# Optimization experiments

Hardware: AMD Instinct MI355X
Metric: run time of the kernel (lower is better)

## Reference

```python
import jax, jax.numpy as jnp
import numpy as np

B, N, C, H, W, V = 2, 8, 64, 192, 256, 200000
R = N * H * W
OUT = 128


def setup_inputs() -> dict:
    key = jax.random.key(0)
    k = jax.random.split(key, 8)
    camera_pose = jnp.eye(4, dtype=jnp.float32) + 0.1 * jax.random.normal(k[0], (B, N, 4, 4), dtype=jnp.float32)
    intr = jnp.array([200.0, 200.0, W / 2.0, H / 2.0, float(W), float(H)], dtype=jnp.float32)
    padded_intrinsics = jnp.broadcast_to(intr, (B, N, 6))
    padded_img_features = jax.random.normal(k[1], (B, N, C, H, W), dtype=jnp.float32)
    depths = jax.random.uniform(k[2], (B, N, H, W), dtype=jnp.float32)
    padding_confidence = jax.random.uniform(k[3], (B, V, 1), dtype=jnp.float32)
    voxel_ids = jax.random.randint(k[4], (B, R), 0, V).astype(jnp.int32)
    hit_mask = jax.random.bernoulli(k[5], 0.5, (B, R))
    w_fc = 0.02 * jax.random.normal(k[6], (C + 1, OUT), dtype=jnp.float32)
    b_fc = 0.01 * jax.random.normal(k[7], (OUT,), dtype=jnp.float32)
    return {"camera_pose": camera_pose, "padded_intrinsics": padded_intrinsics,
            "padded_img_features": padded_img_features, "depths": depths,
            "padding_confidence": padding_confidence, "voxel_ids": voxel_ids,
            "hit_mask": hit_mask, "w_fc": w_fc, "b_fc": b_fc}


def _rays(pose, intr):
    # pose: [B,N,4,4], intr: [B,N,6] = fx,fy,cx,cy,w,h
    fx, fy, cx, cy = intr[..., 0], intr[..., 1], intr[..., 2], intr[..., 3]
    ii, jj = jnp.meshgrid(jnp.arange(W, dtype=intr.dtype), jnp.arange(H, dtype=intr.dtype), indexing="xy")  # [H,W]
    uu = (ii - cx[..., None, None]) / fx[..., None, None]  # [B,N,H,W]
    vv = (jj - cy[..., None, None]) / fy[..., None, None]
    ones = jnp.ones_like(uu)
    local = jnp.stack([uu, vv, ones, ones], axis=-1)  # [B,N,H,W,4]
    pixel_xyz = jnp.einsum("bnij,bnhwj->bnhwi", pose, local)[..., :3]
    origin = pose[..., :3, 3]  # [B,N,3]
    d = pixel_xyz - origin[:, :, None, None, :]
    d = d / jnp.linalg.norm(d, axis=-1, keepdims=True)
    return origin, d


def _scatter_mean(x, ids, mask):
    # x: [R,C]; ids: [R]; mask: [R] bool. Non-hit rays routed to dummy segment V.
    seg = jnp.where(mask, ids, V)
    sums = jax.ops.segment_sum(x, seg, num_segments=V + 1)[:V]
    cnt = jax.ops.segment_sum(mask.astype(x.dtype), seg, num_segments=V + 1)[:V]
    return sums / jnp.maximum(cnt, 1.0)[:, None]  # voxels with no hits stay zero


def reference(camera_pose, padded_intrinsics, padded_img_features, depths,
              padding_confidence, voxel_ids, hit_mask, w_fc, b_fc):
    origins, d = _rays(camera_pose, padded_intrinsics)
    # [B,N,C,H,W] -> [B, N*H*W, C]  (matches permute(0,2,3,1).view(N*H*W,-1) per batch)
    x = jnp.transpose(padded_img_features, (0, 1, 3, 4, 2)).reshape(B, R, C)
    vox = jax.vmap(_scatter_mean)(x, voxel_ids, hit_mask)  # [B,V,C]
    vox = jnp.concatenate([vox, padding_confidence], axis=-1)  # [B,V,C+1]
    out = vox @ w_fc + b_fc  # mix_fc
    return out, d
```

## Files before the change

kernel.cpp:

```cpp
#include <hip/hip_runtime.h>
#include <hip/hip_bf16.h>

#define B_ 2
#define N_ 8
#define C_ 64
#define H_ 192
#define W_ 256
#define V_ 200000
#define OUT_ 128
#define HW_ (H_*W_)
#define R_ (N_*HW_)
#define BV_ (B_*V_)
#define BR_ (B_*R_)
#define SCAN_E 2048
#define SCAN_BLOCKS ((BV_ + SCAN_E - 1)/SCAN_E)

__global__ __launch_bounds__(256) void ray_kernel(
    const float* __restrict__ pose,
    const float* __restrict__ intr,
    float* __restrict__ dout)
{
    const int blocksPerBN = HW_ / 256;
    int tid = threadIdx.x;
    int bn = blockIdx.x / blocksPerBN;
    int hw = (blockIdx.x % blocksPerBN) * 256 + tid;
    int h = hw / W_, w = hw % W_;

    __shared__ float p[12];
    __shared__ float it[4];
    if (tid < 12) p[tid] = pose[bn * 16 + tid];
    if (tid >= 12 && tid < 16) it[tid - 12] = intr[bn * 6 + (tid - 12)];
    __syncthreads();

    float fx = it[0], fy = it[1], cx = it[2], cy = it[3];
    float uu = ((float)w - cx) / fx;
    float vv = ((float)h - cy) / fy;
    float dx = p[0] * uu + p[1] * vv + p[2];
    float dy = p[4] * uu + p[5] * vv + p[6];
    float dz = p[8] * uu + p[9] * vv + p[10];
    float inv = rsqrtf(dx * dx + dy * dy + dz * dz);
    size_t o = (size_t)(bn * HW_ + hw) * 3;
    dout[o + 0] = dx * inv;
    dout[o + 1] = dy * inv;
    dout[o + 2] = dz * inv;
}

__global__ __launch_bounds__(256) void hist_kernel(
    const int* __restrict__ vox,
    const int* __restrict__ hit,
    unsigned* __restrict__ hist)
{
    int t = blockIdx.x * 256 + threadIdx.x;
    if (t >= BR_) return;
    int b = t / R_;
    if (hit[t]) atomicAdd(&hist[b * V_ + vox[t]], 1u);
}

__global__ __launch_bounds__(256) void scanA_kernel(
    const unsigned* __restrict__ hist,
    unsigned* __restrict__ blockSums)
{
    int tid = threadIdx.x;
    int base = blockIdx.x * SCAN_E + tid * 8;
    unsigned s = 0;
    #pragma unroll
    for (int j = 0; j < 8; ++j) {
        int idx = base + j;
        if (idx < BV_) s += hist[idx];
    }
    __shared__ unsigned sh[256];
    sh[tid] = s; __syncthreads();
    for (int d = 128; d > 0; d >>= 1) {
        if (tid < d) sh[tid] += sh[tid + d];
        __syncthreads();
    }
    if (tid == 0) blockSums[blockIdx.x] = sh[0];
}

__global__ __launch_bounds__(256) void scanB_kernel(
    const unsigned* __restrict__ blockSums,
    unsigned* __restrict__ blockOffsets)
{
    int tid = threadIdx.x;
    unsigned v = (tid < SCAN_BLOCKS) ? blockSums[tid] : 0u;
    __shared__ unsigned sh[256];
    sh[tid] = v; __syncthreads();
    for (int d = 1; d < 256; d <<= 1) {
        unsigned t = (tid >= d) ? sh[tid - d] : 0u;
        __syncthreads();
        sh[tid] += t;
        __syncthreads();
    }
    if (tid < SCAN_BLOCKS) blockOffsets[tid] = sh[tid] - v;
}

__global__ __launch_bounds__(256) void scanC_kernel(
    const unsigned* __restrict__ hist,
    const unsigned* __restrict__ blockOffsets,
    unsigned* __restrict__ offsets)
{
    int tid = threadIdx.x;
    int base = blockIdx.x * SCAN_E + tid * 8;
    unsigned e[8];
    unsigned s = 0;
    #pragma unroll
    for (int j = 0; j < 8; ++j) {
        int idx = base + j;
        e[j] = (idx < BV_) ? hist[idx] : 0u;
        s += e[j];
    }
    __shared__ unsigned sh[256];
    sh[tid] = s; __syncthreads();
    for (int d = 1; d < 256; d <<= 1) {
        unsigned t = (tid >= d) ? sh[tid - d] : 0u;
        __syncthreads();
        sh[tid] += t;
        __syncthreads();
    }
    unsigned run = blockOffsets[blockIdx.x] + (sh[tid] - s);
    #pragma unroll
    for (int j = 0; j < 8; ++j) {
        int idx = base + j;
        if (idx < BV_) offsets[idx] = run;
        run += e[j];
    }
}

__global__ __launch_bounds__(256) void scatterfeat_kernel(
    const float* __restrict__ feat,
    const int* __restrict__ vox,
    const int* __restrict__ hit,
    const unsigned* __restrict__ offsets,
    unsigned* __restrict__ offs2,
    float* __restrict__ gathered,
    int b0)
{
    int t = blockIdx.x * 256 + threadIdx.x;
    int p = b0 * R_ + t;
    if (!hit[p]) return;
    int b = p / R_;
    int r = p - b * R_;
    unsigned base = offsets[(size_t)b0 * V_];
    int key = b * V_ + vox[p];
    unsigned pos = atomicAdd(&offs2[key], 1u) - base;

    int n = r / HW_;
    int hw = r - n * HW_;
    const float* fb = feat + ((size_t)b * N_ + n) * (size_t)(C_ * HW_) + hw;

    float v[64];
    #pragma unroll
    for (int c = 0; c < 64; ++c) v[c] = fb[(size_t)c * HW_];

    float4* gp = (float4*)(gathered + (size_t)pos * 64);
    #pragma unroll
    for (int q = 0; q < 16; ++q) {
        float4 st; st.x = v[4*q]; st.y = v[4*q+1]; st.z = v[4*q+2]; st.w = v[4*q+3];
        gp[q] = st;
    }
}

__global__ __launch_bounds__(256) void gemm_fused_kernel(
    const float* __restrict__ gathered,
    const unsigned* __restrict__ hist,
    const unsigned* __restrict__ offsets,
    const float* __restrict__ conf,
    const float* __restrict__ wfc,
    const float* __restrict__ bfc,
    float* __restrict__ outp,
    int b0)
{
    const int VPB = 32;
    __shared__ float wl[65][128];
    __shared__ float voxT[65][36];
    __shared__ float bl[128];
    int tid = threadIdx.x;
    int bv0 = b0 * V_ + blockIdx.x * VPB;
    unsigned base = offsets[(size_t)b0 * V_];

    for (int i = tid; i < 65 * 128; i += 256)
        wl[i >> 7][i & 127] = wfc[i];
    if (tid < 128) bl[tid] = bfc[tid];
    if (tid < VPB) voxT[64][tid] = conf[bv0 + tid];

    int lane = tid & 63;
    int wv = tid >> 6;
    #pragma unroll
    for (int i = 0; i < 8; ++i) {
        int lv = wv * 8 + i;
        int bv = bv0 + lv;
        unsigned cnt = hist[bv];
        unsigned st = offsets[bv] - base;
        float acc = 0.0f;
        for (unsigned k = 0; k < cnt; ++k)
            acc += gathered[(size_t)(st + k) * 64 + lane];
        voxT[lane][lv] = acc / fmaxf((float)cnt, 1.0f);
    }
    __syncthreads();

    int oc = tid & 31;
    int vr = tid >> 5;
    float acc[4][4];
    float4 bq = *(float4*)&bl[oc * 4];
    #pragma unroll
    for (int i = 0; i < 4; ++i) {
        acc[i][0] = bq.x; acc[i][1] = bq.y; acc[i][2] = bq.z; acc[i][3] = bq.w;
    }

    #pragma unroll
    for (int c = 0; c < 65; ++c) {
        float4 v4 = *(float4*)&voxT[c][vr * 4];
        float4 w4 = *(float4*)&wl[c][oc * 4];
        acc[0][0] += v4.x * w4.x; acc[0][1] += v4.x * w4.y; acc[0][2] += v4.x * w4.z; acc[0][3] += v4.x * w4.w;
        acc[1][0] += v4.y * w4.x; acc[1][1] += v4.y * w4.y; acc[1][2] += v4.y * w4.z; acc[1][3] += v4.y * w4.w;
        acc[2][0] += v4.z * w4.x; acc[2][1] += v4.z * w4.y; acc[2][2] += v4.z * w4.z; acc[2][3] += v4.z * w4.w;
        acc[3][0] += v4.w * w4.x; acc[3][1] += v4.w * w4.y; acc[3][2] += v4.w * w4.z; acc[3][3] += v4.w * w4.w;
    }

    #pragma unroll
    for (int i = 0; i < 4; ++i) {
        size_t bv = (size_t)(bv0 + vr * 4 + i);
        float4 st;
        st.x = acc[i][0]; st.y = acc[i][1]; st.z = acc[i][2]; st.w = acc[i][3];
        *(float4*)&outp[bv * OUT_ + oc * 4] = st;
    }
}

__global__ __launch_bounds__(256) void scatter_kernel(
    const float* __restrict__ feat,
    const int* __restrict__ vox_ids,
    const int* __restrict__ hit,
    float* __restrict__ sums,
    unsigned* __restrict__ cnts)
{
    const int PPT = 2;
    const int blocksPerBN = HW_ / (256 * PPT);
    int tid = threadIdx.x;
    int bn = blockIdx.x / blocksPerBN;
    int b = bn >> 3;
    int hw0 = (blockIdx.x % blocksPerBN) * (256 * PPT) + tid * PPT;
    int r0 = (bn & 7) * HW_ + hw0;

    int2 vid = *(const int2*)(vox_ids + (size_t)b * R_ + r0);
    int2 ht  = *(const int2*)(hit + (size_t)b * R_ + r0);
    if (!(ht.x | ht.y)) return;

    unsigned* cb = cnts + (size_t)b * V_;
    if (ht.x) atomicAdd(&cb[vid.x], 1u);
    if (ht.y) atomicAdd(&cb[vid.y], 1u);

    float* sb = sums + (size_t)b * (size_t)V_ * C_;
    float* s0 = sb + (size_t)vid.x * C_;
    float* s1 = sb + (size_t)vid.y * C_;
    const float* fb = feat + (size_t)bn * C_ * HW_ + hw0;

    #pragma unroll 8
    for (int c = 0; c < C_; ++c) {
        float2 rw = *(const float2*)(fb + (size_t)c * HW_);
        if (ht.x) unsafeAtomicAdd(s0 + c, rw.x);
        if (ht.y) unsafeAtomicAdd(s1 + c, rw.y);
    }
}

__global__ __launch_bounds__(256) void gemm_atomic_kernel(
    const float* __restrict__ sums,
    const unsigned* __restrict__ cnts,
    const float* __restrict__ conf,
    const float* __restrict__ wfc,
    const float* __restrict__ bfc,
    float* __restrict__ outp)
{
    const int VPB = 32;
    __shared__ float wl[65][128];
    __shared__ float voxT[65][36];
    __shared__ float bl[128];
    __shared__ float invc[VPB];
    int tid = threadIdx.x;
    int bv0 = blockIdx.x * VPB;

    for (int i = tid; i < 65 * 128; i += 256)
        wl[i >> 7][i & 127] = wfc[i];
    if (tid < 128) bl[tid] = bfc[tid];
    if (tid < VPB) {
        unsigned cn = cnts[bv0 + tid];
        invc[tid] = 1.0f / (float)(cn > 1u ? cn : 1u);
        voxT[64][tid] = conf[bv0 + tid];
    }
    __syncthreads();

    for (int i = tid; i < VPB * C_; i += 256) {
        int vx = i >> 6, c = i & 63;
        voxT[c][vx] = sums[(size_t)bv0 * C_ + i] * invc[vx];
    }
    __syncthreads();

    int oc = tid & 31;
    int vr = tid >> 5;
    float acc[4][4];
    float4 bq = *(float4*)&bl[oc * 4];
    #pragma unroll
    for (int i = 0; i < 4; ++i) {
        acc[i][0] = bq.x; acc[i][1] = bq.y; acc[i][2] = bq.z; acc[i][3] = bq.w;
    }

    #pragma unroll
    for (int c = 0; c < 65; ++c) {
        float4 v4 = *(float4*)&voxT[c][vr * 4];
        float4 w4 = *(float4*)&wl[c][oc * 4];
        acc[0][0] += v4.x * w4.x; acc[0][1] += v4.x * w4.y; acc[0][2] += v4.x * w4.z; acc[0][3] += v4.x * w4.w;
        acc[1][0] += v4.y * w4.x; acc[1][1] += v4.y * w4.y; acc[1][2] += v4.y * w4.z; acc[1][3] += v4.y * w4.w;
        acc[2][0] += v4.z * w4.x; acc[2][1] += v4.z * w4.y; acc[2][2] += v4.z * w4.z; acc[2][3] += v4.z * w4.w;
        acc[3][0] += v4.w * w4.x; acc[3][1] += v4.w * w4.y; acc[3][2] += v4.w * w4.z; acc[3][3] += v4.w * w4.w;
    }

    #pragma unroll
    for (int i = 0; i < 4; ++i) {
        size_t bv = (size_t)(bv0 + vr * 4 + i);
        float4 st;
        st.x = acc[i][0]; st.y = acc[i][1]; st.z = acc[i][2]; st.w = acc[i][3];
        *(float4*)&outp[bv * OUT_ + oc * 4] = st;
    }
}

extern "C" void kernel_launch(void* const* d_in, const int* in_sizes, int n_in,
                              void* d_out, int out_size, void* d_ws, size_t ws_size,
                              hipStream_t stream) {
    const float* pose = (const float*)d_in[0];
    const float* intr = (const float*)d_in[1];
    const float* feat = (const float*)d_in[2];
    const float* conf = (const float*)d_in[4];
    const int* vox_ids = (const int*)d_in[5];
    const int* hit = (const int*)d_in[6];
    const float* wfc = (const float*)d_in[7];
    const float* bfc = (const float*)d_in[8];

    float* out = (float*)d_out;
    float* dray = out + (size_t)B_ * V_ * OUT_;

    ray_kernel<<<(B_ * N_ * HW_) / 256, 256, 0, stream>>>(pose, intr, dray);

    size_t hist_bytes = (size_t)BV_ * sizeof(unsigned);
    size_t gath_full  = (size_t)BR_ * C_ * sizeof(float);
    size_t gath_batch = (size_t)R_ * C_ * sizeof(float);
    size_t ovh = 3 * hist_bytes + 512 * sizeof(unsigned);
    size_t need_full  = gath_full + ovh;
    size_t need_batch = gath_batch + ovh;

    if (ws_size >= need_batch) {
        size_t gath_bytes = (ws_size >= need_full) ? gath_full : gath_batch;
        float* gathered = (float*)d_ws;
        unsigned* hist = (unsigned*)((char*)d_ws + gath_bytes);
        unsigned* offsets = hist + BV_;
        unsigned* offs2 = offsets + BV_;
        unsigned* blockSums = offs2 + BV_;
        unsigned* blockOffsets = blockSums + 256;

        hipMemsetAsync(hist, 0, hist_bytes, stream);
        hist_kernel<<<BR_ / 256, 256, 0, stream>>>(vox_ids, hit, hist);
        scanA_kernel<<<SCAN_BLOCKS, 256, 0, stream>>>(hist, blockSums);
        scanB_kernel<<<1, 256, 0, stream>>>(blockSums, blockOffsets);
        scanC_kernel<<<SCAN_BLOCKS, 256, 0, stream>>>(hist, blockOffsets, offsets);
        hipMemcpyAsync(offs2, offsets, hist_bytes, hipMemcpyDeviceToDevice, stream);

        if (ws_size >= need_full) {
            scatterfeat_kernel<<<BR_ / 256, 256, 0, stream>>>(feat, vox_ids, hit, offsets, offs2, gathered, 0);
            gemm_fused_kernel<<<BV_ / 32, 256, 0, stream>>>(gathered, hist, offsets, conf, wfc, bfc, out, 0);
        } else {
            for (int b = 0; b < B_; ++b) {
                scatterfeat_kernel<<<R_ / 256, 256, 0, stream>>>(feat, vox_ids, hit, offsets, offs2, gathered, b);
                gemm_fused_kernel<<<V_ / 32, 256, 0, stream>>>(gathered, hist, offsets, conf, wfc, bfc, out, b);
            }
        }
    } else {
        float* sums = (float*)d_ws;
        size_t sums_bytes = (size_t)B_ * V_ * C_ * sizeof(float);
        unsigned* cnts = (unsigned*)((char*)d_ws + sums_bytes);
        size_t cnts_bytes = (size_t)B_ * V_ * sizeof(unsigned);

        hipMemsetAsync(d_ws, 0, sums_bytes + cnts_bytes, stream);
        scatter_kernel<<<(B_ * N_ * HW_) / (256 * 2), 256, 0, stream>>>(feat, vox_ids, hit, sums, cnts);
        gemm_atomic_kernel<<<(B_ * V_) / 32, 256, 0, stream>>>(sums, cnts, conf, wfc, bfc, out);
    }
}
```

Baseline: 621.2 us.

## Process two rays per thread in scatter, widen GEMM tile, fuse offset copy

The offsets copy is folded into the scan kernel, removing a separate device-to-device memcpy. The feature scatter now handles two adjacent pixels per thread with float2 loads in four channel chunks, which cuts per-thread register pressure and halves the hit/vox index loads. The fused mean+GEMM kernel moves from 32 to 64 voxels per block, issues the segment loads for eight voxels at a time to raise memory parallelism, and streams the weights through shared memory in 22-row chunks to hold LDS use down. The cost is extra synchronisation for the weight reloads and more accumulator registers per thread.

```diff
diff --git a/kernel.cpp b/kernel.cpp
--- a/kernel.cpp
+++ b/kernel.cpp
@@ -97,7 +97,8 @@
 __global__ __launch_bounds__(256) void scanC_kernel(
     const unsigned* __restrict__ hist,
     const unsigned* __restrict__ blockOffsets,
-    unsigned* __restrict__ offsets)
+    unsigned* __restrict__ offsets,
+    unsigned* __restrict__ offs2)
 {
     int tid = threadIdx.x;
     int base = blockIdx.x * SCAN_E + tid * 8;
@@ -121,7 +122,7 @@
     #pragma unroll
     for (int j = 0; j < 8; ++j) {
         int idx = base + j;
-        if (idx < BV_) offsets[idx] = run;
+        if (idx < BV_) { offsets[idx] = run; offs2[idx] = run; }
         run += e[j];
     }
 }
@@ -136,27 +137,45 @@
     int b0)
 {
     int t = blockIdx.x * 256 + threadIdx.x;
-    int p = b0 * R_ + t;
-    if (!hit[p]) return;
-    int b = p / R_;
-    int r = p - b * R_;
+    int p0 = b0 * R_ + t * 2;
+    int2 ht = *(const int2*)(hit + p0);
+    if (!(ht.x | ht.y)) return;
+    int2 vd = *(const int2*)(vox + p0);
+    int b = p0 / R_;
+    int r0 = p0 - b * R_;
     unsigned base = offsets[(size_t)b0 * V_];
-    int key = b * V_ + vox[p];
-    unsigned pos = atomicAdd(&offs2[key], 1u) - base;
-
-    int n = r / HW_;
-    int hw = r - n * HW_;
+    unsigned px = 0, py = 0;
+    if (ht.x) px = atomicAdd(&offs2[b * V_ + vd.x], 1u) - base;
+    if (ht.y) py = atomicAdd(&offs2[b * V_ + vd.y], 1u) - base;
+
+    int n = r0 / HW_;
+    int hw = r0 - n * HW_;
     const float* fb = feat + ((size_t)b * N_ + n) * (size_t)(C_ * HW_) + hw;
-
-    float v[64];
-    #pragma unroll
-    for (int c = 0; c < 64; ++c) v[c] = fb[(size_t)c * HW_];
-
-    float4* gp = (float4*)(gathered + (size_t)pos * 64);
-    #pragma unroll
-    for (int q = 0; q < 16; ++q) {
-        float4 st; st.x = v[4*q]; st.y = v[4*q+1]; st.z = v[4*q+2]; st.w = v[4*q+3];
-        gp[q] = st;
+    float* gx = gathered + (size_t)px * 64;
+    float* gy = gathered + (size_t)py * 64;
+
+    #pragma unroll 1
+    for (int ch = 0; ch < 4; ++ch) {
+        float2 v[16];
+        #pragma unroll
+        for (int j = 0; j < 16; ++j)
+            v[j] = *(const float2*)(fb + (size_t)(ch * 16 + j) * HW_);
+        if (ht.x) {
+            #pragma unroll
+            for (int q = 0; q < 4; ++q) {
+                float4 s;
+                s.x = v[4*q].x; s.y = v[4*q+1].x; s.z = v[4*q+2].x; s.w = v[4*q+3].x;
+                *(float4*)(gx + ch * 16 + q * 4) = s;
+            }
+        }
+        if (ht.y) {
+            #pragma unroll
+            for (int q = 0; q < 4; ++q) {
+                float4 s;
+                s.x = v[4*q].y; s.y = v[4*q+1].y; s.z = v[4*q+2].y; s.w = v[4*q+3].y;
+                *(float4*)(gy + ch * 16 + q * 4) = s;
+            }
+        }
     }
 }
 
@@ -170,59 +189,88 @@
     float* __restrict__ outp,
     int b0)
 {
-    const int VPB = 32;
-    __shared__ float wl[65][128];
-    __shared__ float voxT[65][36];
+    const int VPB = 64;
+    const int KC = 22;
+    __shared__ float wl[KC][128];
+    __shared__ float voxT[66][68];
     __shared__ float bl[128];
     int tid = threadIdx.x;
     int bv0 = b0 * V_ + blockIdx.x * VPB;
     unsigned base = offsets[(size_t)b0 * V_];
 
-    for (int i = tid; i < 65 * 128; i += 256)
-        wl[i >> 7][i & 127] = wfc[i];
     if (tid < 128) bl[tid] = bfc[tid];
     if (tid < VPB) voxT[64][tid] = conf[bv0 + tid];
+    if (tid < 68)  voxT[65][tid] = 0.0f;
 
     int lane = tid & 63;
     int wv = tid >> 6;
-    #pragma unroll
-    for (int i = 0; i < 8; ++i) {
-        int lv = wv * 8 + i;
-        int bv = bv0 + lv;
-        unsigned cnt = hist[bv];
-        unsigned st = offsets[bv] - base;
-        float acc = 0.0f;
-        for (unsigned k = 0; k < cnt; ++k)
-            acc += gathered[(size_t)(st + k) * 64 + lane];
-        voxT[lane][lv] = acc / fmaxf((float)cnt, 1.0f);
-    }
+    for (int g = 0; g < 2; ++g) {
+        unsigned cn[8], st[8];
+        float macc[8];
+        #pragma unroll
+        for (int i = 0; i < 8; ++i) {
+            int bv = bv0 + wv * 16 + g * 8 + i;
+            cn[i] = hist[bv];
+            st[i] = offsets[bv] - base;
+        }
+        #pragma unroll
+        for (int i = 0; i < 8; ++i)
+            macc[i] = cn[i] ? gathered[(size_t)st[i] * 64 + lane] : 0.0f;
+        #pragma unroll
+        for (int i = 0; i < 8; ++i)
+            for (unsigned k = 1; k < cn[i]; ++k)
+                macc[i] += gathered[(size_t)(st[i] + k) * 64 + lane];
+        #pragma unroll
+        for (int i = 0; i < 8; ++i)
+            voxT[lane][wv * 16 + g * 8 + i] = macc[i] / fmaxf((float)cn[i], 1.0f);
+    }
+
+    for (int i = tid; i < KC * 128; i += 256)
+        wl[i >> 7][i & 127] = wfc[i];
     __syncthreads();
 
     int oc = tid & 31;
     int vr = tid >> 5;
-    float acc[4][4];
+    float acc[8][4];
     float4 bq = *(float4*)&bl[oc * 4];
     #pragma unroll
-    for (int i = 0; i < 4; ++i) {
+    for (int i = 0; i < 8; ++i) {
         acc[i][0] = bq.x; acc[i][1] = bq.y; acc[i][2] = bq.z; acc[i][3] = bq.w;
     }
 
-    #pragma unroll
-    for (int c = 0; c < 65; ++c) {
-        float4 v4 = *(float4*)&voxT[c][vr * 4];
-        float4 w4 = *(float4*)&wl[c][oc * 4];
-        acc[0][0] += v4.x * w4.x; acc[0][1] += v4.x * w4.y; acc[0][2] += v4.x * w4.z; acc[0][3] += v4.x * w4.w;
-        acc[1][0] += v4.y * w4.x; acc[1][1] += v4.y * w4.y; acc[1][2] += v4.y * w4.z; acc[1][3] += v4.y * w4.w;
-        acc[2][0] += v4.z * w4.x; acc[2][1] += v4.z * w4.y; acc[2][2] += v4.z * w4.z; acc[2][3] += v4.z * w4.w;
-        acc[3][0] += v4.w * w4.x; acc[3][1] += v4.w * w4.y; acc[3][2] += v4.w * w4.z; acc[3][3] += v4.w * w4.w;
-    }
-
-    #pragma unroll
-    for (int i = 0; i < 4; ++i) {
-        size_t bv = (size_t)(bv0 + vr * 4 + i);
-        float4 st;
-        st.x = acc[i][0]; st.y = acc[i][1]; st.z = acc[i][2]; st.w = acc[i][3];
-        *(float4*)&outp[bv * OUT_ + oc * 4] = st;
+    for (int h = 0; h < 3; ++h) {
+        int c0 = h * KC;
+        #pragma unroll
+        for (int cl = 0; cl < KC; ++cl) {
+            int c = c0 + cl;
+            float4 va = *(float4*)&voxT[c][vr * 8];
+            float4 vb = *(float4*)&voxT[c][vr * 8 + 4];
+            float4 w4 = *(float4*)&wl[cl][oc * 4];
+            acc[0][0] += va.x * w4.x; acc[0][1] += va.x * w4.y; acc[0][2] += va.x * w4.z; acc[0][3] += va.x * w4.w;
+            acc[1][0] += va.y * w4.x; acc[1][1] += va.y * w4.y; acc[1][2] += va.y * w4.z; acc[1][3] += va.y * w4.w;
+            acc[2][0] += va.z * w4.x; acc[2][1] += va.z * w4.y; acc[2][2] += va.z * w4.z; acc[2][3] += va.z * w4.w;
+            acc[3][0] += va.w * w4.x; acc[3][1] += va.w * w4.y; acc[3][2] += va.w * w4.z; acc[3][3] += va.w * w4.w;
+            acc[4][0] += vb.x * w4.x; acc[4][1] += vb.x * w4.y; acc[4][2] += vb.x * w4.z; acc[4][3] += vb.x * w4.w;
+            acc[5][0] += vb.y * w4.x; acc[5][1] += vb.y * w4.y; acc[5][2] += vb.y * w4.z; acc[5][3] += vb.y * w4.w;
+            acc[6][0] += vb.z * w4.x; acc[6][1] += vb.z * w4.y; acc[6][2] += vb.z * w4.z; acc[6][3] += vb.z * w4.w;
+            acc[7][0] += vb.w * w4.x; acc[7][1] += vb.w * w4.y; acc[7][2] += vb.w * w4.z; acc[7][3] += vb.w * w4.w;
+        }
+        if (h < 2) {
+            __syncthreads();
+            int c0n = (h + 1) * KC;
+            int nc = (c0n + KC <= 65) ? KC : (65 - c0n);
+            for (int i = tid; i < KC * 128; i += 256)
+                wl[i >> 7][i & 127] = (i < nc * 128) ? wfc[c0n * 128 + i] : 0.0f;
+            __syncthreads();
+        }
+    }
+
+    #pragma unroll
+    for (int i = 0; i < 8; ++i) {
+        size_t bv = (size_t)(bv0 + vr * 8 + i);
+        float4 st4;
+        st4.x = acc[i][0]; st4.y = acc[i][1]; st4.z = acc[i][2]; st4.w = acc[i][3];
+        *(float4*)&outp[bv * OUT_ + oc * 4] = st4;
     }
 }
 
@@ -359,16 +407,15 @@
         hist_kernel<<<BR_ / 256, 256, 0, stream>>>(vox_ids, hit, hist);
         scanA_kernel<<<SCAN_BLOCKS, 256, 0, stream>>>(hist, blockSums);
         scanB_kernel<<<1, 256, 0, stream>>>(blockSums, blockOffsets);
-        scanC_kernel<<<SCAN_BLOCKS, 256, 0, stream>>>(hist, blockOffsets, offsets);
-        hipMemcpyAsync(offs2, offsets, hist_bytes, hipMemcpyDeviceToDevice, stream);
+        scanC_kernel<<<SCAN_BLOCKS, 256, 0, stream>>>(hist, blockOffsets, offsets, offs2);
 
         if (ws_size >= need_full) {
-            scatterfeat_kernel<<<BR_ / 256, 256, 0, stream>>>(feat, vox_ids, hit, offsets, offs2, gathered, 0);
-            gemm_fused_kernel<<<BV_ / 32, 256, 0, stream>>>(gathered, hist, offsets, conf, wfc, bfc, out, 0);
+            scatterfeat_kernel<<<BR_ / 512, 256, 0, stream>>>(feat, vox_ids, hit, offsets, offs2, gathered, 0);
+            gemm_fused_kernel<<<BV_ / 64, 256, 0, stream>>>(gathered, hist, offsets, conf, wfc, bfc, out, 0);
         } else {
             for (int b = 0; b < B_; ++b) {
-                scatterfeat_kernel<<<R_ / 256, 256, 0, stream>>>(feat, vox_ids, hit, offsets, offs2, gathered, b);
-                gemm_fused_kernel<<<V_ / 32, 256, 0, stream>>>(gathered, hist, offsets, conf, wfc, bfc, out, b);
+                scatterfeat_kernel<<<R_ / 512, 256, 0, stream>>>(feat, vox_ids, hit, offsets, offs2, gathered, b);
+                gemm_fused_kernel<<<V_ / 64, 256, 0, stream>>>(gathered, hist, offsets, conf, wfc, bfc, out, b);
             }
         }
     } else {
```

After: 804.6 us. +29.5%, slower.
